# Performance work log

Measured on AMD Instinct MI355X. Metric: run time of the kernel, lower is better.

Reference implementation:

```python
import jax, jax.numpy as jnp
import numpy as np

B, L, D, K = 4, 512, 768, 96
H = 4 * D  # projection hidden width


def _proj(x, w1, b1, w2, b2):
    # create_projection_layer: Linear -> ReLU -> (Dropout, identity at eval) -> Linear
    return jnp.maximum(x @ w1 + b1, 0.0) @ w2 + b2


def setup_inputs() -> dict:
    key = jax.random.key(0)
    ks = jax.random.split(key, 12)
    g = lambda k, shape, fan: jax.random.normal(k, shape, jnp.float32) * (1.0 / np.sqrt(fan))
    inp = {
        "h": jax.random.normal(ks[0], (B, L, D), jnp.float32),
        "span_idx": jax.random.randint(ks[1], (B, K, 2), 0, L),
        "ps_w1": g(ks[2], (D, H), D), "ps_b1": jnp.zeros((H,), jnp.float32),
        "ps_w2": g(ks[3], (H, D), H), "ps_b2": jnp.zeros((D,), jnp.float32),
        "pe_w1": g(ks[4], (D, H), D), "pe_b1": jnp.zeros((H,), jnp.float32),
        "pe_w2": g(ks[5], (H, D), H), "pe_b2": jnp.zeros((D,), jnp.float32),
        "so_w1": g(ks[6], (2 * D, H), 2 * D), "so_b1": jnp.zeros((H,), jnp.float32),
        "so_w2": g(ks[7], (H, D), H), "so_b2": jnp.zeros((D,), jnp.float32),
        "ro_w1": g(ks[8], (2 * D, H), 2 * D), "ro_b1": jnp.zeros((H,), jnp.float32),
        "ro_w2": g(ks[9], (H, D), H), "ro_b2": jnp.zeros((D,), jnp.float32),
    }
    return inp


def _gather_tokens(rep, idx):
    # rep: [B,L,D], idx: [B,K] -> [B,K,D]
    b, k = idx.shape
    d = rep.shape[-1]
    return jnp.take_along_axis(rep, jnp.broadcast_to(idx[:, :, None], (b, k, d)), axis=1)


def reference(h, span_idx, ps_w1, ps_b1, ps_w2, ps_b2, pe_w1, pe_b1, pe_w2, pe_b2,
              so_w1, so_b1, so_w2, so_b2, ro_w1, ro_b1, ro_w2, ro_b2):
    # SpanMarkerV1
    start_rep = _proj(h, ps_w1, ps_b1, ps_w2, ps_b2)   # [B,L,D]
    end_rep = _proj(h, pe_w1, pe_b1, pe_w2, pe_b2)     # [B,L,D]
    st = _gather_tokens(start_rep, span_idx[:, :, 0])  # [B,K,D]
    en = _gather_tokens(end_rep, span_idx[:, :, 1])    # [B,K,D]
    cat = jnp.maximum(jnp.concatenate([st, en], axis=-1), 0.0)  # relu
    entity_reps = _proj(cat, so_w1, so_b1, so_w2, so_b2)        # [B,K,D]

    # off-diagonal pair enumeration, row-major (i,j) with i != j — static indices
    n = entity_reps.shape[1]
    idx = np.arange(n)
    ii = np.repeat(idx, n)
    jj = np.tile(idx, n)
    keep = ii != jj
    ii, jj = ii[keep], jj[keep]  # each length n*(n-1)
    pairs = jnp.concatenate([entity_reps[:, ii], entity_reps[:, jj]], axis=-1)  # [B,P,2D]
    return _proj(pairs, ro_w1, ro_b1, ro_w2, ro_b2)  # [B,P,D]
```

## Files before the change

### kernel.cpp

```cpp
#include <hip/hip_runtime.h>
#include <hip/hip_bf16.h>

#define Bdim 4
#define Ldim 512
#define Ddim 768
#define Kspan 96
#define Hdim 3072
#define Pdim 9120
#define MROWS 384
#define NKT4 48

typedef __bf16 bf16x8 __attribute__((ext_vector_type(8)));
typedef float f32x4 __attribute__((ext_vector_type(4)));
typedef float f32x16 __attribute__((ext_vector_type(16)));
typedef unsigned short ushort8v __attribute__((ext_vector_type(8)));

static __device__ __forceinline__ unsigned short f2bf(float x){
  return __builtin_bit_cast(unsigned short, (__bf16)x);
}
static __device__ __forceinline__ float bf2f(unsigned short u){
  return (float)__builtin_bit_cast(__bf16, u);
}
static __device__ __forceinline__ float bfbits2f(unsigned short u){
  return __builtin_bit_cast(float, (unsigned)u << 16);
}

struct TJob { const float* W; unsigned short* Th; unsigned short* Tl; int K; int N; int base; };
struct TJobs { TJob j[7]; };

__global__ __launch_bounds__(256) void transpose_multi(TJobs JJ)
{
  int x = blockIdx.x;
  int ji = 0;
  #pragma unroll
  for (int q = 1; q < 7; q++) if (x >= JJ.j[q].base) ji = q;
  TJob J = JJ.j[ji];
  int local = x - J.base;
  int tilesX = J.N >> 6;
  int bx = local % tilesX, by = local / tilesX;
  __shared__ float tile[64][65];
  int k0 = by * 64, n0 = bx * 64;
  int c = threadIdx.x & 63, r0 = threadIdx.x >> 6;
  for (int p = 0; p < 16; p++){
    int r = r0 + p * 4;
    tile[c][r] = J.W[(size_t)(k0 + r) * J.N + n0 + c];
  }
  __syncthreads();
  for (int p = 0; p < 16; p++){
    int n = r0 + p * 4;
    float xv = tile[n][c];
    unsigned short h = f2bf(xv);
    size_t o = (size_t)(n0 + n) * J.K + k0 + c;
    J.Th[o] = h;
    J.Tl[o] = f2bf(xv - bf2f(h));
  }
}

__global__ __launch_bounds__(256) void pack_w2(
    const float* __restrict__ W, unsigned short* __restrict__ W2P)
{
  __shared__ float tile[64][193];
  int kt = blockIdx.x, nq = blockIdx.y, t = threadIdx.x;
  for (int q = 0; q < 48; q++){
    int flat = q * 256 + t;
    int ks = flat / 192, n = flat - ks * 192;
    tile[ks][n] = W[(size_t)(kt * 64 + ks) * Ddim + nq * 192 + n];
  }
  __syncthreads();
  unsigned short* outp = W2P + (size_t)(nq * 48 + kt) * 12288;
  for (int q = 0; q < 48; q++){
    int o = q * 256 + t;
    int n = o >> 6, kph = o & 63;
    int ks = kph ^ ((n & 7) << 3);
    outp[o] = f2bf(tile[ks][n]);
  }
}

__global__ __launch_bounds__(256) void pack_v(
    const float* __restrict__ Vbuf, unsigned short* __restrict__ Vp)
{
  int kt = blockIdx.x, b = blockIdx.y, t = threadIdx.x;
  unsigned short* outp = Vp + (size_t)(b * 48 + kt) * 6144;
  #pragma unroll
  for (int q = 0; q < 3; q++){
    int item = q * 256 + t;
    int j = item >> 3, g = item & 7;
    const float* src = Vbuf + (size_t)(b * 96 + j) * Hdim + kt * 64 + g * 8;
    f32x4 a0 = *(const f32x4*)src, a1 = *(const f32x4*)(src + 4);
    ushort8v pk;
    #pragma unroll
    for (int e = 0; e < 4; e++) pk[e] = f2bf(a0[e]);
    #pragma unroll
    for (int e = 0; e < 4; e++) pk[e + 4] = f2bf(a1[e]);
    *(ushort8v*)(outp + j * 64 + ((g ^ (j & 7)) << 3)) = pk;
  }
}

__global__ __launch_bounds__(256) void gather_rows(
    const float* __restrict__ h, const int* __restrict__ span, float* __restrict__ hg)
{
  int x = blockIdx.x;
  int sel = (x >= MROWS) ? 1 : 0;
  int r = x - sel * MROWS;
  int b = r / Kspan, k = r - b * Kspan;
  int idx = span[(b * Kspan + k) * 2 + sel];
  const float* src = h + ((size_t)b * Ldim + idx) * Ddim;
  float* dst = hg + (size_t)x * Ddim;
  for (int d = threadIdx.x; d < Ddim; d += 256) dst[d] = src[d];
}

struct GJob {
  const float* A;
  const unsigned short* Wh;
  const unsigned short* Wl;
  const float* bias;
  float* C;
};

template<int MODE, int SPLIT>
__global__ __launch_bounds__(256) void gemm_ms(
    GJob j0, GJob j1, int ldA, int ldW, int ldC, int kLen, size_t csz)
{
  constexpr int SR = 40;
  __shared__ __align__(16) unsigned short Ah[64 * SR], Al[64 * SR];
  __shared__ __align__(16) unsigned short Bh[128 * SR], Bl[128 * SR];
  int zj, s;
  if (SPLIT == 1){ zj = blockIdx.z; s = 0; }
  else { zj = blockIdx.z / SPLIT; s = blockIdx.z % SPLIT; }
  const GJob J = zj ? j1 : j0;
  int kBegin = s * kLen;
  float* Cptr = (MODE == 2) ? (J.C + (size_t)s * csz) : J.C;

  int m0 = blockIdx.y * 64, n0 = blockIdx.x * 128;
  int t = threadIdx.x, lane = t & 63, wid = t >> 6;
  int wm = wid >> 1, wn = wid & 1;
  int lr = lane & 15, lk = (lane >> 4) * 8;
  f32x4 acc[2][4] = {};
  int ar = t >> 2, akq = t & 3;
  for (int k0 = 0; k0 < kLen; k0 += 32){
    {
      const float* sp = J.A + (size_t)(m0 + ar) * ldA + kBegin + k0 + akq * 8;
      f32x4 x0 = *(const f32x4*)sp, x1 = *(const f32x4*)(sp + 4);
      ushort8v vh, vl;
      for (int e = 0; e < 4; e++){ float x = x0[e]; unsigned short hh = f2bf(x); vh[e] = hh; vl[e] = f2bf(x - bf2f(hh)); }
      for (int e = 0; e < 4; e++){ float x = x1[e]; unsigned short hh = f2bf(x); vh[e+4] = hh; vl[e+4] = f2bf(x - bf2f(hh)); }
      *(ushort8v*)&Ah[ar * SR + akq * 8] = vh;
      *(ushort8v*)&Al[ar * SR + akq * 8] = vl;
    }
    for (int p = 0; p < 2; p++){
      int idx = p * 256 + t; int n = idx >> 2, kq = idx & 3;
      size_t go = (size_t)(n0 + n) * ldW + kBegin + k0 + kq * 8;
      *(ushort8v*)&Bh[n * SR + kq * 8] = *(const ushort8v*)(J.Wh + go);
      *(ushort8v*)&Bl[n * SR + kq * 8] = *(const ushort8v*)(J.Wl + go);
    }
    __syncthreads();
    bf16x8 ah[2], al2[2], bh[4], bl[4];
    for (int f = 0; f < 2; f++){ int o = (wm * 32 + f * 16 + lr) * SR + lk; ah[f] = *(const bf16x8*)&Ah[o]; al2[f] = *(const bf16x8*)&Al[o]; }
    for (int g = 0; g < 4; g++){ int o = (wn * 64 + g * 16 + lr) * SR + lk; bh[g] = *(const bf16x8*)&Bh[o]; bl[g] = *(const bf16x8*)&Bl[o]; }
    for (int f = 0; f < 2; f++)
      for (int g = 0; g < 4; g++){
        acc[f][g] = __builtin_amdgcn_mfma_f32_16x16x32_bf16(ah[f],  bh[g], acc[f][g], 0, 0, 0);
        acc[f][g] = __builtin_amdgcn_mfma_f32_16x16x32_bf16(ah[f],  bl[g], acc[f][g], 0, 0, 0);
        acc[f][g] = __builtin_amdgcn_mfma_f32_16x16x32_bf16(al2[f], bh[g], acc[f][g], 0, 0, 0);
      }
    __syncthreads();
  }
  int rr = (lane >> 4) * 4;
  for (int f = 0; f < 2; f++){
    int gm = m0 + wm * 32 + f * 16 + rr;
    for (int g = 0; g < 4; g++){
      int gn = n0 + wn * 64 + g * 16 + (lane & 15);
      float bv = (MODE != 2 && J.bias) ? J.bias[gn] : 0.f;
      for (int r2 = 0; r2 < 4; r2++){
        float v = acc[f][g][r2] + bv;
        if (MODE == 0) v = fmaxf(v, 0.f);
        Cptr[(size_t)(gm + r2) * ldC + gn] = v;
      }
    }
  }
}

template<bool RELU>
__global__ __launch_bounds__(256) void reduce_part(
    const float* __restrict__ P, int S,
    const float* __restrict__ bias0, const float* __restrict__ bias1,
    float* __restrict__ outp, int zCount, int ldOut)
{
  const int MN = MROWS * Ddim;
  int idx4 = blockIdx.x * 256 + threadIdx.x;
  int flat = idx4 * 4;
  if (flat >= MN * zCount) return;
  int z = flat / MN; int rem = flat - z * MN;
  int r = rem / Ddim; int c = rem - r * Ddim;
  const float* base = P + (size_t)z * S * MN + rem;
  f32x4 sv = *(const f32x4*)base;
  for (int ss = 1; ss < S; ss++){ f32x4 v = *(const f32x4*)(base + (size_t)ss * MN); sv += v; }
  const float* bp = z ? bias1 : bias0;
  f32x4 bv = *(const f32x4*)(bp + c);
  sv += bv;
  if (RELU) for (int e = 0; e < 4; e++) sv[e] = fmaxf(sv[e], 0.f);
  *(f32x4*)(outp + (size_t)r * ldOut + z * Ddim + c) = sv;
}

__global__ __launch_bounds__(256, 2) void pair_gemm4(
    const float* __restrict__ U,
    const unsigned short* __restrict__ Vp,
    const unsigned short* __restrict__ W2P,
    const float* __restrict__ b2,
    float* __restrict__ out)
{
  __shared__ __align__(16) unsigned short Bs[2][12288];
  __shared__ __align__(16) unsigned short Vs[2][6144];

  int x = blockIdx.x;
  int xcd = x & 7;
  int s = x >> 3;
  int combo = xcd + ((s >= 48) ? 8 : 0);
  int ig = (s >= 48) ? (s - 48) : s;
  int nq = combo & 3, b = combo >> 2;

  int t = threadIdx.x, lane = t & 63, w = t >> 6;
  int wm = w >> 1, wn = w & 1;
  int l31 = lane & 31, hsel = lane >> 5;
  int i = ig * 2 + wm;
  const float* Urow = U + ((size_t)(b * 96 + i)) * Hdim + hsel * 8;

  f32x16 acc[3][3] = {};

  auto issueB = [&](int kt, int buf){
    const unsigned short* srcb = W2P + (size_t)(nq * 48 + kt) * 12288 + t * 8;
    #pragma unroll
    for (int q = 0; q < 6; q++){
      __builtin_amdgcn_global_load_lds(
          (const __attribute__((address_space(1))) unsigned int*)(srcb + q * 2048),
          (__attribute__((address_space(3))) unsigned int*)&Bs[buf][q * 2048 + t * 8],
          16, 0, 0);
    }
  };
  auto issueV = [&](int kt, int buf){
    const unsigned short* srcv = Vp + (size_t)(b * 48 + kt) * 6144 + t * 8;
    #pragma unroll
    for (int q = 0; q < 3; q++){
      __builtin_amdgcn_global_load_lds(
          (const __attribute__((address_space(1))) unsigned int*)(srcv + q * 2048),
          (__attribute__((address_space(3))) unsigned int*)&Vs[buf][q * 2048 + t * 8],
          16, 0, 0);
    }
  };

  issueB(0, 0);
  issueV(0, 0);
  __syncthreads();

  for (int kt = 0; kt < NKT4; kt++){
    int cur = kt & 1;
    if (kt + 1 < NKT4){ issueB(kt + 1, cur ^ 1); issueV(kt + 1, cur ^ 1); }

    float uf[4][8];
    {
      const float* ub = Urow + kt * 64;
      #pragma unroll
      for (int kh = 0; kh < 4; kh++){
        *(f32x4*)&uf[kh][0] = *(const f32x4*)(ub + kh * 16);
        *(f32x4*)&uf[kh][4] = *(const f32x4*)(ub + kh * 16 + 4);
      }
    }

    #pragma unroll
    for (int kh = 0; kh < 4; kh++){
      int gx16 = (kh * 2 + hsel) * 16;
      bf16x8 bfr[3], afr[3];
      #pragma unroll
      for (int nf = 0; nf < 3; nf++){
        int n = wn * 96 + nf * 32 + l31;
        bfr[nf] = *(const bf16x8*)((const char*)&Bs[cur][0] + n * 128 + (gx16 ^ ((n & 7) << 4)));
      }
      #pragma unroll
      for (int mf = 0; mf < 3; mf++){
        int j = mf * 32 + l31;
        ushort8v vv = *(const ushort8v*)((const char*)&Vs[cur][0] + j * 128 + (gx16 ^ ((j & 7) << 4)));
        ushort8v pk;
        #pragma unroll
        for (int e = 0; e < 8; e++)
          pk[e] = f2bf(fmaxf(uf[kh][e] + bfbits2f(vv[e]), 0.f));
        afr[mf] = __builtin_bit_cast(bf16x8, pk);
      }
      __builtin_amdgcn_s_setprio(1);
      #pragma unroll
      for (int mf = 0; mf < 3; mf++)
        #pragma unroll
        for (int nf = 0; nf < 3; nf++)
          acc[mf][nf] = __builtin_amdgcn_mfma_f32_32x32x16_bf16(afr[mf], bfr[nf], acc[mf][nf], 0, 0, 0);
      __builtin_amdgcn_s_setprio(0);
    }
    __syncthreads();
  }

  size_t outB = (size_t)b * Pdim;
  int colbase = nq * 192 + wn * 96;
  float bc[3];
  #pragma unroll
  for (int nf = 0; nf < 3; nf++) bc[nf] = b2[colbase + nf * 32 + l31];
  #pragma unroll
  for (int mf = 0; mf < 3; mf++){
    #pragma unroll
    for (int reg = 0; reg < 16; reg++){
      int j = mf * 32 + (reg & 3) + 8 * (reg >> 2) + 4 * hsel;
      if (j == i) continue;
      int p = i * 95 + j - (j > i ? 1 : 0);
      float* orow = out + (outB + p) * Ddim + colbase;
      #pragma unroll
      for (int nf = 0; nf < 3; nf++)
        orow[nf * 32 + l31] = acc[mf][nf][reg] + bc[nf];
    }
  }
}

extern "C" void kernel_launch(void* const* d_in, const int* in_sizes, int n_in,
                              void* d_out, int out_size, void* d_ws, size_t ws_size,
                              hipStream_t stream)
{
  (void)in_sizes; (void)n_in; (void)out_size;
  const float* h     = (const float*)d_in[0];
  const int*   span  = (const int*)d_in[1];
  const float* ps_w1 = (const float*)d_in[2];
  const float* ps_b1 = (const float*)d_in[3];
  const float* ps_w2 = (const float*)d_in[4];
  const float* ps_b2 = (const float*)d_in[5];
  const float* pe_w1 = (const float*)d_in[6];
  const float* pe_b1 = (const float*)d_in[7];
  const float* pe_w2 = (const float*)d_in[8];
  const float* pe_b2 = (const float*)d_in[9];
  const float* so_w1 = (const float*)d_in[10];
  const float* so_b1 = (const float*)d_in[11];
  const float* so_w2 = (const float*)d_in[12];
  const float* so_b2 = (const float*)d_in[13];
  const float* ro_w1 = (const float*)d_in[14];
  const float* ro_b1 = (const float*)d_in[15];
  const float* ro_w2 = (const float*)d_in[16];
  const float* ro_b2 = (const float*)d_in[17];

  char* ws = (char*)d_ws;
  size_t off = 0;
  auto alloc_us = [&](size_t n)->unsigned short*{
    unsigned short* p = (unsigned short*)(ws + off);
    off += ((n * 2 + 255) & ~(size_t)255);
    return p;
  };
  auto alloc_f = [&](size_t n)->float*{
    float* p = (float*)(ws + off);
    off += ((n * 4 + 255) & ~(size_t)255);
    return p;
  };

  unsigned short* ps1h = alloc_us((size_t)Hdim * Ddim); unsigned short* ps1l = alloc_us((size_t)Hdim * Ddim);
  unsigned short* ps2h = alloc_us((size_t)Ddim * Hdim); unsigned short* ps2l = alloc_us((size_t)Ddim * Hdim);
  unsigned short* pe1h = alloc_us((size_t)Hdim * Ddim); unsigned short* pe1l = alloc_us((size_t)Hdim * Ddim);
  unsigned short* pe2h = alloc_us((size_t)Ddim * Hdim); unsigned short* pe2l = alloc_us((size_t)Ddim * Hdim);
  unsigned short* so1h = alloc_us((size_t)Hdim * 2 * Ddim); unsigned short* so1l = alloc_us((size_t)Hdim * 2 * Ddim);
  unsigned short* so2h = alloc_us((size_t)Ddim * Hdim); unsigned short* so2l = alloc_us((size_t)Ddim * Hdim);
  unsigned short* ro1h = alloc_us((size_t)Hdim * 2 * Ddim); unsigned short* ro1l = alloc_us((size_t)Hdim * 2 * Ddim);
  unsigned short* W2P  = alloc_us((size_t)4 * 48 * 12288);
  unsigned short* Vp   = alloc_us((size_t)4 * 48 * 6144);
  float* hg     = alloc_f((size_t)2 * MROWS * Ddim);
  float* mid_s  = alloc_f((size_t)MROWS * Hdim);
  float* mid_e  = alloc_f((size_t)MROWS * Hdim);
  float* cat    = alloc_f((size_t)MROWS * 2 * Ddim);
  float* entity = alloc_f((size_t)MROWS * Ddim);
  float* Ubuf   = alloc_f((size_t)MROWS * Hdim);
  float* Vbuf   = alloc_f((size_t)MROWS * Hdim);
  const size_t MN = (size_t)MROWS * Ddim;
  float* P2 = alloc_f(8 * MN);
  float* P3 = alloc_f(4 * MN);
  if (off > ws_size) return;

  dim3 tb(256);

  {
    TJobs JJ;
    int base = 0;
    auto add = [&](int idx, const float* W, unsigned short* Th, unsigned short* Tl, int K, int N){
      JJ.j[idx] = TJob{W, Th, Tl, K, N, base};
      base += (N / 64) * (K / 64);
    };
    add(0, ps_w1, ps1h, ps1l, Ddim, Hdim);
    add(1, ps_w2, ps2h, ps2l, Hdim, Ddim);
    add(2, pe_w1, pe1h, pe1l, Ddim, Hdim);
    add(3, pe_w2, pe2h, pe2l, Hdim, Ddim);
    add(4, so_w1, so1h, so1l, 2 * Ddim, Hdim);
    add(5, so_w2, so2h, so2l, Hdim, Ddim);
    add(6, ro_w1, ro1h, ro1l, 2 * Ddim, Hdim);
    transpose_multi<<<base, tb, 0, stream>>>(JJ);
  }
  pack_w2<<<dim3(NKT4, 4), tb, 0, stream>>>(ro_w2, W2P);

  gather_rows<<<2 * MROWS, tb, 0, stream>>>(h, span, hg);

  {
    GJob j0{hg,                      ps1h, ps1l, ps_b1, mid_s};
    GJob j1{hg + (size_t)MROWS*Ddim, pe1h, pe1l, pe_b1, mid_e};
    gemm_ms<0,1><<<dim3(Hdim/128, MROWS/64, 2), tb, 0, stream>>>(j0, j1, Ddim, Ddim, Hdim, Ddim, 0);
  }
  {
    GJob j0{mid_s, ps2h, ps2l, nullptr, P2};
    GJob j1{mid_e, pe2h, pe2l, nullptr, P2 + 4*MN};
    gemm_ms<2,4><<<dim3(Ddim/128, MROWS/64, 8), tb, 0, stream>>>(j0, j1, Hdim, Hdim, Ddim, Hdim/4, MN);
  }
  reduce_part<true><<<(2*(int)MN)/1024, tb, 0, stream>>>(P2, 4, ps_b2, pe_b2, cat, 2, 2*Ddim);
  {
    GJob j0{cat, so1h, so1l, so_b1, mid_s};
    gemm_ms<0,1><<<dim3(Hdim/128, MROWS/64, 1), tb, 0, stream>>>(j0, j0, 2*Ddim, 2*Ddim, Hdim, 2*Ddim, 0);
  }
  {
    GJob j0{mid_s, so2h, so2l, nullptr, P3};
    gemm_ms<2,4><<<dim3(Ddim/128, MROWS/64, 4), tb, 0, stream>>>(j0, j0, Hdim, Hdim, Ddim, Hdim/4, MN);
  }
  reduce_part<false><<<((int)MN)/1024, tb, 0, stream>>>(P3, 4, so_b2, so_b2, entity, 1, Ddim);
  {
    GJob j0{entity, ro1h,        ro1l,        ro_b1,   Ubuf};
    GJob j1{entity, ro1h + Ddim, ro1l + Ddim, nullptr, Vbuf};
    gemm_ms<1,1><<<dim3(Hdim/128, MROWS/64, 2), tb, 0, stream>>>(j0, j1, Ddim, 2*Ddim, Hdim, Ddim, 0);
  }
  pack_v<<<dim3(NKT4, Bdim), tb, 0, stream>>>(Vbuf, Vp);

  pair_gemm4<<<768, tb, 0, stream>>>(Ubuf, Vp, W2P, ro_b2, (float*)d_out);
}
```

Baseline: 470.7 us.

## Narrow pair GEMM N-tile to 128 columns and software-pipeline V fragment loads

The final pair GEMM now splits the 768 output columns into six 128-wide tiles instead of four 192-wide ones. That gives 1152 blocks, lowers accumulator register use per wave, and shrinks the B shared-memory buffer. The inner k-loop is unrolled into macro steps that prefetch the next V fragments from LDS while the current ones are converted and fed to MFMA, and the setprio hints are dropped. In exchange, the activated A fragments (relu(U+V)) are rebuilt more times overall, and U/V traffic grows with the extra column tiles.

New measurement: 502.4 us. 6.7% more time.

```diff
diff --git a/kernel.cpp b/kernel.cpp
--- a/kernel.cpp
+++ b/kernel.cpp
@@ -59,16 +59,16 @@
 __global__ __launch_bounds__(256) void pack_w2(
     const float* __restrict__ W, unsigned short* __restrict__ W2P)
 {
-  __shared__ float tile[64][193];
+  __shared__ float tile[64][129];
   int kt = blockIdx.x, nq = blockIdx.y, t = threadIdx.x;
-  for (int q = 0; q < 48; q++){
+  for (int q = 0; q < 32; q++){
     int flat = q * 256 + t;
-    int ks = flat / 192, n = flat - ks * 192;
-    tile[ks][n] = W[(size_t)(kt * 64 + ks) * Ddim + nq * 192 + n];
+    int ks = flat >> 7, n = flat & 127;
+    tile[ks][n] = W[(size_t)(kt * 64 + ks) * Ddim + nq * 128 + n];
   }
   __syncthreads();
-  unsigned short* outp = W2P + (size_t)(nq * 48 + kt) * 12288;
-  for (int q = 0; q < 48; q++){
+  unsigned short* outp = W2P + (size_t)(nq * 48 + kt) * 8192;
+  for (int q = 0; q < 32; q++){
     int o = q * 256 + t;
     int n = o >> 6, kph = o & 63;
     int ks = kph ^ ((n & 7) << 3);
@@ -202,22 +202,57 @@
   *(f32x4*)(outp + (size_t)r * ldOut + z * Ddim + c) = sv;
 }
 
-__global__ __launch_bounds__(256, 2) void pair_gemm4(
+#define KH_STEP(KH, VVC, VVN, UA, UB, PRE) { \
+  bf16x8 bfr[2]; \
+  int gx = ((KH) * 2 + hsel) * 16; \
+  _Pragma("unroll") \
+  for (int nf = 0; nf < 2; nf++){ \
+    int n = wn * 64 + nf * 32 + l31; \
+    bfr[nf] = *(const bf16x8*)((const char*)&Bs[cur][0] + n * 128 + (gx ^ ((n & 7) << 4))); \
+  } \
+  if (PRE){ \
+    int gn = (((KH) + 1) * 2 + hsel) * 16; \
+    _Pragma("unroll") \
+    for (int mf = 0; mf < 3; mf++){ \
+      int j = mf * 32 + l31; \
+      VVN[mf] = *(const bf16x8*)((const char*)&Vs[cur][0] + j * 128 + (gn ^ ((j & 7) << 4))); \
+    } \
+  } \
+  bf16x8 afr[3]; \
+  _Pragma("unroll") \
+  for (int mf = 0; mf < 3; mf++){ \
+    ushort8v vb = __builtin_bit_cast(ushort8v, VVC[mf]); \
+    ushort8v pk; \
+    _Pragma("unroll") \
+    for (int e = 0; e < 4; e++) pk[e]   = f2bf(fmaxf(UA[e] + bfbits2f(vb[e]),   0.f)); \
+    _Pragma("unroll") \
+    for (int e = 0; e < 4; e++) pk[e+4] = f2bf(fmaxf(UB[e] + bfbits2f(vb[e+4]), 0.f)); \
+    afr[mf] = __builtin_bit_cast(bf16x8, pk); \
+  } \
+  _Pragma("unroll") \
+  for (int mf = 0; mf < 3; mf++) \
+    _Pragma("unroll") \
+    for (int nf = 0; nf < 2; nf++) \
+      acc[mf][nf] = __builtin_amdgcn_mfma_f32_32x32x16_bf16(afr[mf], bfr[nf], acc[mf][nf], 0, 0, 0); \
+}
+
+__global__ __launch_bounds__(256, 2) void pair_gemm5(
     const float* __restrict__ U,
     const unsigned short* __restrict__ Vp,
     const unsigned short* __restrict__ W2P,
     const float* __restrict__ b2,
     float* __restrict__ out)
 {
-  __shared__ __align__(16) unsigned short Bs[2][12288];
+  __shared__ __align__(16) unsigned short Bs[2][8192];
   __shared__ __align__(16) unsigned short Vs[2][6144];
 
   int x = blockIdx.x;
   int xcd = x & 7;
   int s = x >> 3;
-  int combo = xcd + ((s >= 48) ? 8 : 0);
-  int ig = (s >= 48) ? (s - 48) : s;
-  int nq = combo & 3, b = combo >> 2;
+  int grp = s / 48;
+  int ig  = s - grp * 48;
+  int combo = xcd + grp * 8;
+  int nq = combo % 6, b = combo / 6;
 
   int t = threadIdx.x, lane = t & 63, w = t >> 6;
   int wm = w >> 1, wn = w & 1;
@@ -225,82 +260,65 @@
   int i = ig * 2 + wm;
   const float* Urow = U + ((size_t)(b * 96 + i)) * Hdim + hsel * 8;
 
-  f32x16 acc[3][3] = {};
-
-  auto issueB = [&](int kt, int buf){
-    const unsigned short* srcb = W2P + (size_t)(nq * 48 + kt) * 12288 + t * 8;
-    #pragma unroll
-    for (int q = 0; q < 6; q++){
-      __builtin_amdgcn_global_load_lds(
-          (const __attribute__((address_space(1))) unsigned int*)(srcb + q * 2048),
-          (__attribute__((address_space(3))) unsigned int*)&Bs[buf][q * 2048 + t * 8],
-          16, 0, 0);
-    }
-  };
-  auto issueV = [&](int kt, int buf){
-    const unsigned short* srcv = Vp + (size_t)(b * 48 + kt) * 6144 + t * 8;
-    #pragma unroll
-    for (int q = 0; q < 3; q++){
-      __builtin_amdgcn_global_load_lds(
-          (const __attribute__((address_space(1))) unsigned int*)(srcv + q * 2048),
-          (__attribute__((address_space(3))) unsigned int*)&Vs[buf][q * 2048 + t * 8],
-          16, 0, 0);
-    }
-  };
-
-  issueB(0, 0);
-  issueV(0, 0);
+  f32x16 acc[3][2] = {};
+
+  const unsigned short* srcB0 = W2P + (size_t)(nq * 48) * 8192 + t * 8;
+  const unsigned short* srcV0 = Vp  + (size_t)(b  * 48) * 6144 + t * 8;
+
+  #pragma unroll
+  for (int q = 0; q < 4; q++)
+    __builtin_amdgcn_global_load_lds(
+        (const __attribute__((address_space(1))) unsigned int*)(srcB0 + q * 2048),
+        (__attribute__((address_space(3))) unsigned int*)&Bs[0][q * 2048 + t * 8], 16, 0, 0);
+  #pragma unroll
+  for (int q = 0; q < 3; q++)
+    __builtin_amdgcn_global_load_lds(
+        (const __attribute__((address_space(1))) unsigned int*)(srcV0 + q * 2048),
+        (__attribute__((address_space(3))) unsigned int*)&Vs[0][q * 2048 + t * 8], 16, 0, 0);
   __syncthreads();
 
   for (int kt = 0; kt < NKT4; kt++){
     int cur = kt & 1;
-    if (kt + 1 < NKT4){ issueB(kt + 1, cur ^ 1); issueV(kt + 1, cur ^ 1); }
-
-    float uf[4][8];
+    bf16x8 vvA[3], vvB[3];
     {
-      const float* ub = Urow + kt * 64;
-      #pragma unroll
-      for (int kh = 0; kh < 4; kh++){
-        *(f32x4*)&uf[kh][0] = *(const f32x4*)(ub + kh * 16);
-        *(f32x4*)&uf[kh][4] = *(const f32x4*)(ub + kh * 16 + 4);
-      }
-    }
-
-    #pragma unroll
-    for (int kh = 0; kh < 4; kh++){
-      int gx16 = (kh * 2 + hsel) * 16;
-      bf16x8 bfr[3], afr[3];
-      #pragma unroll
-      for (int nf = 0; nf < 3; nf++){
-        int n = wn * 96 + nf * 32 + l31;
-        bfr[nf] = *(const bf16x8*)((const char*)&Bs[cur][0] + n * 128 + (gx16 ^ ((n & 7) << 4)));
-      }
+      int g0 = hsel * 16;
       #pragma unroll
       for (int mf = 0; mf < 3; mf++){
         int j = mf * 32 + l31;
-        ushort8v vv = *(const ushort8v*)((const char*)&Vs[cur][0] + j * 128 + (gx16 ^ ((j & 7) << 4)));
-        ushort8v pk;
-        #pragma unroll
-        for (int e = 0; e < 8; e++)
-          pk[e] = f2bf(fmaxf(uf[kh][e] + bfbits2f(vv[e]), 0.f));
-        afr[mf] = __builtin_bit_cast(bf16x8, pk);
+        vvA[mf] = *(const bf16x8*)((const char*)&Vs[cur][0] + j * 128 + (g0 ^ ((j & 7) << 4)));
       }
-      __builtin_amdgcn_s_setprio(1);
+    }
+    const float* ub = Urow + kt * 64;
+    f32x4 u00 = *(const f32x4*)(ub +  0), u01 = *(const f32x4*)(ub +  4);
+    f32x4 u10 = *(const f32x4*)(ub + 16), u11 = *(const f32x4*)(ub + 20);
+    f32x4 u20 = *(const f32x4*)(ub + 32), u21 = *(const f32x4*)(ub + 36);
+    f32x4 u30 = *(const f32x4*)(ub + 48), u31 = *(const f32x4*)(ub + 52);
+    if (kt + 1 < NKT4){
+      const unsigned short* sB = srcB0 + (size_t)(kt + 1) * 8192;
+      const unsigned short* sV = srcV0 + (size_t)(kt + 1) * 6144;
       #pragma unroll
-      for (int mf = 0; mf < 3; mf++)
-        #pragma unroll
-        for (int nf = 0; nf < 3; nf++)
-          acc[mf][nf] = __builtin_amdgcn_mfma_f32_32x32x16_bf16(afr[mf], bfr[nf], acc[mf][nf], 0, 0, 0);
-      __builtin_amdgcn_s_setprio(0);
-    }
+      for (int q = 0; q < 4; q++)
+        __builtin_amdgcn_global_load_lds(
+            (const __attribute__((address_space(1))) unsigned int*)(sB + q * 2048),
+            (__attribute__((address_space(3))) unsigned int*)&Bs[cur ^ 1][q * 2048 + t * 8], 16, 0, 0);
+      #pragma unroll
+      for (int q = 0; q < 3; q++)
+        __builtin_amdgcn_global_load_lds(
+            (const __attribute__((address_space(1))) unsigned int*)(sV + q * 2048),
+            (__attribute__((address_space(3))) unsigned int*)&Vs[cur ^ 1][q * 2048 + t * 8], 16, 0, 0);
+    }
+    KH_STEP(0, vvA, vvB, u00, u01, 1)
+    KH_STEP(1, vvB, vvA, u10, u11, 1)
+    KH_STEP(2, vvA, vvB, u20, u21, 1)
+    KH_STEP(3, vvB, vvA, u30, u31, 0)
     __syncthreads();
   }
 
   size_t outB = (size_t)b * Pdim;
-  int colbase = nq * 192 + wn * 96;
-  float bc[3];
-  #pragma unroll
-  for (int nf = 0; nf < 3; nf++) bc[nf] = b2[colbase + nf * 32 + l31];
+  int colbase = nq * 128 + wn * 64;
+  float bc[2];
+  #pragma unroll
+  for (int nf = 0; nf < 2; nf++) bc[nf] = b2[colbase + nf * 32 + l31];
   #pragma unroll
   for (int mf = 0; mf < 3; mf++){
     #pragma unroll
@@ -310,7 +328,7 @@
       int p = i * 95 + j - (j > i ? 1 : 0);
       float* orow = out + (outB + p) * Ddim + colbase;
       #pragma unroll
-      for (int nf = 0; nf < 3; nf++)
+      for (int nf = 0; nf < 2; nf++)
         orow[nf * 32 + l31] = acc[mf][nf][reg] + bc[nf];
     }
   }
@@ -360,7 +378,7 @@
   unsigned short* so1h = alloc_us((size_t)Hdim * 2 * Ddim); unsigned short* so1l = alloc_us((size_t)Hdim * 2 * Ddim);
   unsigned short* so2h = alloc_us((size_t)Ddim * Hdim); unsigned short* so2l = alloc_us((size_t)Ddim * Hdim);
   unsigned short* ro1h = alloc_us((size_t)Hdim * 2 * Ddim); unsigned short* ro1l = alloc_us((size_t)Hdim * 2 * Ddim);
-  unsigned short* W2P  = alloc_us((size_t)4 * 48 * 12288);
+  unsigned short* W2P  = alloc_us((size_t)6 * 48 * 8192);
   unsigned short* Vp   = alloc_us((size_t)4 * 48 * 6144);
   float* hg     = alloc_f((size_t)2 * MROWS * Ddim);
   float* mid_s  = alloc_f((size_t)MROWS * Hdim);
@@ -392,7 +410,7 @@
     add(6, ro_w1, ro1h, ro1l, 2 * Ddim, Hdim);
     transpose_multi<<<base, tb, 0, stream>>>(JJ);
   }
-  pack_w2<<<dim3(NKT4, 4), tb, 0, stream>>>(ro_w2, W2P);
+  pack_w2<<<dim3(NKT4, 6), tb, 0, stream>>>(ro_w2, W2P);
 
   gather_rows<<<2 * MROWS, tb, 0, stream>>>(h, span, hg);
 
@@ -418,10 +436,10 @@
   reduce_part<false><<<((int)MN)/1024, tb, 0, stream>>>(P3, 4, so_b2, so_b2, entity, 1, Ddim);
   {
     GJob j0{entity, ro1h,        ro1l,        ro_b1,   Ubuf};
-    GJob j1{entity, ro1h + Ddim, ro1l + Ddim, nullptr, Vbuf};
+    GJob j1{entity, ro1h + Ddim, ro1l + Ddim, 2*Ddim == 0 ? nullptr : nullptr, Vbuf};
     gemm_ms<1,1><<<dim3(Hdim/128, MROWS/64, 2), tb, 0, stream>>>(j0, j1, Ddim, 2*Ddim, Hdim, Ddim, 0);
   }
   pack_v<<<dim3(NKT4, Bdim), tb, 0, stream>>>(Vbuf, Vp);
 
-  pair_gemm4<<<768, tb, 0, stream>>>(Ubuf, Vp, W2P, ro_b2, (float*)d_out);
-}
+  pair_gemm5<<<1152, tb, 0, stream>>>(Ubuf, Vp, W2P, ro_b2, (float*)d_out);
+}
```

## Restructure pair GEMM: build A tile once in LDS, retile to 192x128, drop pack_v

Applied to the files above, without the earlier changes.

The pair kernel now builds the relu(U_i + V_j) bf16 A tile cooperatively into LDS once per k-step, instead of having each wave rebuild it from V in registers. It uses K=32 steps with 128-column output tiles over 6 column groups and 1152 blocks, and stages both U rows in LDS. The V projection GEMM writes bf16 directly through a new epilogue mode, which removes the pack_v kernel and the fp32 V buffer. The so_w2 split-K is raised from 4 to 8 partitions. The goal is to remove redundant conversions and a launch and to improve occupancy, at the cost of more LDS traffic and more barriers per k-step.

New measurement: 490.6 us. 4.2% more time.

```diff
diff --git a/kernel.cpp b/kernel.cpp
--- a/kernel.cpp
+++ b/kernel.cpp
@@ -8,7 +8,7 @@
 #define Hdim 3072
 #define Pdim 9120
 #define MROWS 384
-#define NKT4 48
+#define NT6 96
 
 typedef __bf16 bf16x8 __attribute__((ext_vector_type(8)));
 typedef float f32x4 __attribute__((ext_vector_type(4)));
@@ -59,40 +59,20 @@
 __global__ __launch_bounds__(256) void pack_w2(
     const float* __restrict__ W, unsigned short* __restrict__ W2P)
 {
-  __shared__ float tile[64][193];
+  __shared__ float tile[32][129];
   int kt = blockIdx.x, nq = blockIdx.y, t = threadIdx.x;
-  for (int q = 0; q < 48; q++){
+  for (int q = 0; q < 16; q++){
     int flat = q * 256 + t;
-    int ks = flat / 192, n = flat - ks * 192;
-    tile[ks][n] = W[(size_t)(kt * 64 + ks) * Ddim + nq * 192 + n];
+    int kl = flat >> 7, n = flat & 127;
+    tile[kl][n] = W[(size_t)(kt * 32 + kl) * Ddim + nq * 128 + n];
   }
   __syncthreads();
-  unsigned short* outp = W2P + (size_t)(nq * 48 + kt) * 12288;
-  for (int q = 0; q < 48; q++){
+  unsigned short* outp = W2P + (size_t)(nq * 96 + kt) * 4096;
+  for (int q = 0; q < 16; q++){
     int o = q * 256 + t;
-    int n = o >> 6, kph = o & 63;
-    int ks = kph ^ ((n & 7) << 3);
-    outp[o] = f2bf(tile[ks][n]);
-  }
-}
-
-__global__ __launch_bounds__(256) void pack_v(
-    const float* __restrict__ Vbuf, unsigned short* __restrict__ Vp)
-{
-  int kt = blockIdx.x, b = blockIdx.y, t = threadIdx.x;
-  unsigned short* outp = Vp + (size_t)(b * 48 + kt) * 6144;
-  #pragma unroll
-  for (int q = 0; q < 3; q++){
-    int item = q * 256 + t;
-    int j = item >> 3, g = item & 7;
-    const float* src = Vbuf + (size_t)(b * 96 + j) * Hdim + kt * 64 + g * 8;
-    f32x4 a0 = *(const f32x4*)src, a1 = *(const f32x4*)(src + 4);
-    ushort8v pk;
-    #pragma unroll
-    for (int e = 0; e < 4; e++) pk[e] = f2bf(a0[e]);
-    #pragma unroll
-    for (int e = 0; e < 4; e++) pk[e + 4] = f2bf(a1[e]);
-    *(ushort8v*)(outp + j * 64 + ((g ^ (j & 7)) << 3)) = pk;
+    int n = o >> 5, slot = (o >> 3) & 3, e = o & 7;
+    int kl = (slot ^ ((n >> 1) & 3)) * 8 + e;
+    outp[o] = f2bf(tile[kl][n]);
   }
 }
 
@@ -170,11 +150,16 @@
     int gm = m0 + wm * 32 + f * 16 + rr;
     for (int g = 0; g < 4; g++){
       int gn = n0 + wn * 64 + g * 16 + (lane & 15);
-      float bv = (MODE != 2 && J.bias) ? J.bias[gn] : 0.f;
+      float bv = ((MODE == 0 || MODE == 1) && J.bias) ? J.bias[gn] : 0.f;
+      if (MODE == 5 && zj == 0) bv = J.bias[gn];
       for (int r2 = 0; r2 < 4; r2++){
         float v = acc[f][g][r2] + bv;
         if (MODE == 0) v = fmaxf(v, 0.f);
-        Cptr[(size_t)(gm + r2) * ldC + gn] = v;
+        if (MODE == 5 && zj == 1){
+          ((unsigned short*)J.C)[(size_t)(gm + r2) * ldC + gn] = f2bf(v);
+        } else {
+          Cptr[(size_t)(gm + r2) * ldC + gn] = v;
+        }
       }
     }
   }
@@ -202,105 +187,132 @@
   *(f32x4*)(outp + (size_t)r * ldOut + z * Ddim + c) = sv;
 }
 
-__global__ __launch_bounds__(256, 2) void pair_gemm4(
+__global__ __launch_bounds__(256, 2) void pair_gemm7(
     const float* __restrict__ U,
     const unsigned short* __restrict__ Vp,
     const unsigned short* __restrict__ W2P,
     const float* __restrict__ b2,
     float* __restrict__ out)
 {
-  __shared__ __align__(16) unsigned short Bs[2][12288];
-  __shared__ __align__(16) unsigned short Vs[2][6144];
+  __shared__ __align__(16) unsigned short As[2][192 * 32];
+  __shared__ __align__(16) unsigned short Bs[2][128 * 32];
+  __shared__ __align__(16) float Uls[2][Hdim];
 
   int x = blockIdx.x;
   int xcd = x & 7;
   int s = x >> 3;
-  int combo = xcd + ((s >= 48) ? 8 : 0);
-  int ig = (s >= 48) ? (s - 48) : s;
-  int nq = combo & 3, b = combo >> 2;
+  int grp = s / 48;
+  int ig  = s - grp * 48;
+  int combo = xcd + grp * 8;
+  int nq = combo % 6, b = combo / 6;
 
   int t = threadIdx.x, lane = t & 63, w = t >> 6;
   int wm = w >> 1, wn = w & 1;
   int l31 = lane & 31, hsel = lane >> 5;
-  int i = ig * 2 + wm;
-  const float* Urow = U + ((size_t)(b * 96 + i)) * Hdim + hsel * 8;
-
-  f32x16 acc[3][3] = {};
-
+  int i0 = ig * 2, i = i0 + wm;
+
+  int brow = t >> 2, bg = t & 3;
+  int vj[3];
+  #pragma unroll
+  for (int q = 0; q < 3; q++){
+    int r = brow + 64 * q;
+    vj[q] = (r >= 96) ? (r - 96) : r;
+  }
+
+  f32x16 acc[3][2] = {};
+  ushort8v vE[3], vO[3];
+
+  auto loadV = [&](int kt, ushort8v* dst){
+    #pragma unroll
+    for (int q = 0; q < 3; q++)
+      dst[q] = *(const ushort8v*)(Vp + (size_t)(b * 96 + vj[q]) * Hdim + kt * 32 + bg * 8);
+  };
   auto issueB = [&](int kt, int buf){
-    const unsigned short* srcb = W2P + (size_t)(nq * 48 + kt) * 12288 + t * 8;
-    #pragma unroll
-    for (int q = 0; q < 6; q++){
-      __builtin_amdgcn_global_load_lds(
-          (const __attribute__((address_space(1))) unsigned int*)(srcb + q * 2048),
-          (__attribute__((address_space(3))) unsigned int*)&Bs[buf][q * 2048 + t * 8],
-          16, 0, 0);
-    }
-  };
-  auto issueV = [&](int kt, int buf){
-    const unsigned short* srcv = Vp + (size_t)(b * 48 + kt) * 6144 + t * 8;
+    const unsigned short* src = W2P + (size_t)(nq * 96 + kt) * 4096 + t * 8;
+    unsigned short* d0 = (buf == 0) ? &Bs[0][t * 8] : &Bs[1][t * 8];
+    __builtin_amdgcn_global_load_lds(
+        (const __attribute__((address_space(1))) unsigned int*)src,
+        (__attribute__((address_space(3))) unsigned int*)d0, 16, 0, 0);
+    __builtin_amdgcn_global_load_lds(
+        (const __attribute__((address_space(1))) unsigned int*)(src + 2048),
+        (__attribute__((address_space(3))) unsigned int*)(d0 + 2048), 16, 0, 0);
+  };
+  auto build = [&](int kt, int buf, ushort8v* vsrc){
     #pragma unroll
     for (int q = 0; q < 3; q++){
-      __builtin_amdgcn_global_load_lds(
-          (const __attribute__((address_space(1))) unsigned int*)(srcv + q * 2048),
-          (__attribute__((address_space(3))) unsigned int*)&Vs[buf][q * 2048 + t * 8],
-          16, 0, 0);
-    }
-  };
-
-  issueB(0, 0);
-  issueV(0, 0);
-  __syncthreads();
-
-  for (int kt = 0; kt < NKT4; kt++){
-    int cur = kt & 1;
-    if (kt + 1 < NKT4){ issueB(kt + 1, cur ^ 1); issueV(kt + 1, cur ^ 1); }
-
-    float uf[4][8];
-    {
-      const float* ub = Urow + kt * 64;
-      #pragma unroll
-      for (int kh = 0; kh < 4; kh++){
-        *(f32x4*)&uf[kh][0] = *(const f32x4*)(ub + kh * 16);
-        *(f32x4*)&uf[kh][4] = *(const f32x4*)(ub + kh * 16 + 4);
+      int r = brow + 64 * q;
+      int ihalf = (r >= 96) ? 1 : 0;
+      const float* up = &Uls[ihalf][kt * 32 + bg * 8];
+      f32x4 ua = *(const f32x4*)up;
+      f32x4 ub = *(const f32x4*)(up + 4);
+      ushort8v vv = vsrc[q];
+      ushort8v pk;
+      #pragma unroll
+      for (int e = 0; e < 4; e++) pk[e]     = f2bf(fmaxf(ua[e] + bfbits2f(vv[e]),     0.f));
+      #pragma unroll
+      for (int e = 0; e < 4; e++) pk[e + 4] = f2bf(fmaxf(ub[e] + bfbits2f(vv[e + 4]), 0.f));
+      unsigned short* dp = (buf == 0) ? &As[0][0] : &As[1][0];
+      *(ushort8v*)(dp + r * 32 + ((bg ^ ((r >> 1) & 3)) << 3)) = pk;
+    }
+  };
+  auto compute = [&](int buf){
+    const unsigned short* ap = (buf == 0) ? &As[0][0] : &As[1][0];
+    const unsigned short* bp = (buf == 0) ? &Bs[0][0] : &Bs[1][0];
+    #pragma unroll
+    for (int kh = 0; kh < 2; kh++){
+      int g = kh * 2 + hsel;
+      bf16x8 bfr[2], afr[3];
+      #pragma unroll
+      for (int nf = 0; nf < 2; nf++){
+        int n = wn * 64 + nf * 32 + l31;
+        bfr[nf] = *(const bf16x8*)(bp + n * 32 + ((g ^ ((n >> 1) & 3)) << 3));
       }
-    }
-
-    #pragma unroll
-    for (int kh = 0; kh < 4; kh++){
-      int gx16 = (kh * 2 + hsel) * 16;
-      bf16x8 bfr[3], afr[3];
-      #pragma unroll
-      for (int nf = 0; nf < 3; nf++){
-        int n = wn * 96 + nf * 32 + l31;
-        bfr[nf] = *(const bf16x8*)((const char*)&Bs[cur][0] + n * 128 + (gx16 ^ ((n & 7) << 4)));
+      #pragma unroll
+      for (int mf = 0; mf < 3; mf++){
+        int r = wm * 96 + mf * 32 + l31;
+        afr[mf] = *(const bf16x8*)(ap + r * 32 + ((g ^ ((r >> 1) & 3)) << 3));
       }
-      #pragma unroll
-      for (int mf = 0; mf < 3; mf++){
-        int j = mf * 32 + l31;
-        ushort8v vv = *(const ushort8v*)((const char*)&Vs[cur][0] + j * 128 + (gx16 ^ ((j & 7) << 4)));
-        ushort8v pk;
-        #pragma unroll
-        for (int e = 0; e < 8; e++)
-          pk[e] = f2bf(fmaxf(uf[kh][e] + bfbits2f(vv[e]), 0.f));
-        afr[mf] = __builtin_bit_cast(bf16x8, pk);
-      }
-      __builtin_amdgcn_s_setprio(1);
       #pragma unroll
       for (int mf = 0; mf < 3; mf++)
         #pragma unroll
-        for (int nf = 0; nf < 3; nf++)
+        for (int nf = 0; nf < 2; nf++)
           acc[mf][nf] = __builtin_amdgcn_mfma_f32_32x32x16_bf16(afr[mf], bfr[nf], acc[mf][nf], 0, 0, 0);
-      __builtin_amdgcn_s_setprio(0);
-    }
+    }
+  };
+
+  loadV(0, vE);
+  issueB(0, 0);
+  {
+    const float* u0 = U + (size_t)(b * 96 + i0) * Hdim;
+    for (int q = t; q < 2 * (Hdim / 4); q += 256){
+      int r = q / (Hdim / 4), c = q - r * (Hdim / 4);
+      *(f32x4*)&Uls[r][c * 4] = *(const f32x4*)(u0 + (size_t)r * Hdim + c * 4);
+    }
+  }
+  __syncthreads();
+  build(0, 0, vE);
+  loadV(1, vO);
+  __syncthreads();
+
+  for (int kt = 0; kt < NT6; kt += 2){
+    if (kt + 1 < NT6) issueB(kt + 1, 1);
+    if (kt + 2 < NT6) loadV(kt + 2, vE);
+    if (kt + 1 < NT6) build(kt + 1, 1, vO);
+    compute(0);
     __syncthreads();
+    int ko = kt + 1;
+    if (ko + 1 < NT6) issueB(ko + 1, 0);
+    if (ko + 2 < NT6) loadV(ko + 2, vO);
+    if (ko + 1 < NT6) build(ko + 1, 0, vE);
+    compute(1);
+    __syncthreads();
   }
 
   size_t outB = (size_t)b * Pdim;
-  int colbase = nq * 192 + wn * 96;
-  float bc[3];
+  int colbase = nq * 128 + wn * 64;
+  float bc[2];
   #pragma unroll
-  for (int nf = 0; nf < 3; nf++) bc[nf] = b2[colbase + nf * 32 + l31];
+  for (int nf = 0; nf < 2; nf++) bc[nf] = b2[colbase + nf * 32 + l31];
   #pragma unroll
   for (int mf = 0; mf < 3; mf++){
     #pragma unroll
@@ -310,7 +322,7 @@
       int p = i * 95 + j - (j > i ? 1 : 0);
       float* orow = out + (outB + p) * Ddim + colbase;
       #pragma unroll
-      for (int nf = 0; nf < 3; nf++)
+      for (int nf = 0; nf < 2; nf++)
         orow[nf * 32 + l31] = acc[mf][nf][reg] + bc[nf];
     }
   }
@@ -360,18 +372,17 @@
   unsigned short* so1h = alloc_us((size_t)Hdim * 2 * Ddim); unsigned short* so1l = alloc_us((size_t)Hdim * 2 * Ddim);
   unsigned short* so2h = alloc_us((size_t)Ddim * Hdim); unsigned short* so2l = alloc_us((size_t)Ddim * Hdim);
   unsigned short* ro1h = alloc_us((size_t)Hdim * 2 * Ddim); unsigned short* ro1l = alloc_us((size_t)Hdim * 2 * Ddim);
-  unsigned short* W2P  = alloc_us((size_t)4 * 48 * 12288);
-  unsigned short* Vp   = alloc_us((size_t)4 * 48 * 6144);
+  unsigned short* W2P  = alloc_us((size_t)6 * 96 * 4096);
+  unsigned short* Vp   = alloc_us((size_t)MROWS * Hdim);
   float* hg     = alloc_f((size_t)2 * MROWS * Ddim);
   float* mid_s  = alloc_f((size_t)MROWS * Hdim);
   float* mid_e  = alloc_f((size_t)MROWS * Hdim);
   float* cat    = alloc_f((size_t)MROWS * 2 * Ddim);
   float* entity = alloc_f((size_t)MROWS * Ddim);
   float* Ubuf   = alloc_f((size_t)MROWS * Hdim);
-  float* Vbuf   = alloc_f((size_t)MROWS * Hdim);
   const size_t MN = (size_t)MROWS * Ddim;
   float* P2 = alloc_f(8 * MN);
-  float* P3 = alloc_f(4 * MN);
+  float* P3 = alloc_f(8 * MN);
   if (off > ws_size) return;
 
   dim3 tb(256);
@@ -392,7 +403,7 @@
     add(6, ro_w1, ro1h, ro1l, 2 * Ddim, Hdim);
     transpose_multi<<<base, tb, 0, stream>>>(JJ);
   }
-  pack_w2<<<dim3(NKT4, 4), tb, 0, stream>>>(ro_w2, W2P);
+  pack_w2<<<dim3(NT6, 6), tb, 0, stream>>>(ro_w2, W2P);
 
   gather_rows<<<2 * MROWS, tb, 0, stream>>>(h, span, hg);
 
@@ -413,15 +424,14 @@
   }
   {
     GJob j0{mid_s, so2h, so2l, nullptr, P3};
-    gemm_ms<2,4><<<dim3(Ddim/128, MROWS/64, 4), tb, 0, stream>>>(j0, j0, Hdim, Hdim, Ddim, Hdim/4, MN);
-  }
-  reduce_part<false><<<((int)MN)/1024, tb, 0, stream>>>(P3, 4, so_b2, so_b2, entity, 1, Ddim);
-  {
-    GJob j0{entity, ro1h,        ro1l,        ro_b1,   Ubuf};
-    GJob j1{entity, ro1h + Ddim, ro1l + Ddim, nullptr, Vbuf};
-    gemm_ms<1,1><<<dim3(Hdim/128, MROWS/64, 2), tb, 0, stream>>>(j0, j1, Ddim, 2*Ddim, Hdim, Ddim, 0);
-  }
-  pack_v<<<dim3(NKT4, Bdim), tb, 0, stream>>>(Vbuf, Vp);
-
-  pair_gemm4<<<768, tb, 0, stream>>>(Ubuf, Vp, W2P, ro_b2, (float*)d_out);
-}
+    gemm_ms<2,8><<<dim3(Ddim/128, MROWS/64, 8), tb, 0, stream>>>(j0, j0, Hdim, Hdim, Ddim, Hdim/8, MN);
+  }
+  reduce_part<false><<<((int)MN)/1024, tb, 0, stream>>>(P3, 8, so_b2, so_b2, entity, 1, Ddim);
+  {
+    GJob j0{entity, ro1h,        ro1l,        ro_b1,  Ubuf};
+    GJob j1{entity, ro1h + Ddim, ro1l + Ddim, nullptr, (float*)Vp};
+    gemm_ms<5,1><<<dim3(Hdim/128, MROWS/64, 2), tb, 0, stream>>>(j0, j1, Ddim, 2*Ddim, Hdim, Ddim, 0);
+  }
+
+  pair_gemm7<<<1152, tb, 0, stream>>>(Ubuf, Vp, W2P, ro_b2, (float*)d_out);
+}
```
